# Performance work log

Measured on AMD Instinct MI355X. Metric: run time of the kernel, lower is better.

Reference implementation:

```python
import jax, jax.numpy as jnp
import numpy as np
import math

EMBED_DIM = 1024
NUM_HEADS = 16
HEAD_DIM = EMBED_DIM // NUM_HEADS
SEGMENT_LENGTHS = [2048, 4096]
DILATION_RATES = [1, 2]
B, N = 1, 8192
IS_CAUSAL = True


def setup_inputs() -> dict:
    key = jax.random.key(0)
    ks = jax.random.split(key, 12)
    def w(k):
        return (jax.random.normal(k, (EMBED_DIM, EMBED_DIM), dtype=jnp.float32) * 0.02)
    inp = {
        'query': jax.random.normal(ks[0], (B, N, EMBED_DIM), dtype=jnp.float32),
        'key':   jax.random.normal(ks[1], (B, N, EMBED_DIM), dtype=jnp.float32),
        'value': jax.random.normal(ks[2], (B, N, EMBED_DIM), dtype=jnp.float32),
        'Wq': w(ks[3]), 'bq': jnp.zeros((EMBED_DIM,), jnp.float32),
        'Wk': w(ks[4]), 'bk': jnp.zeros((EMBED_DIM,), jnp.float32),
        'Wv': w(ks[5]), 'bv': jnp.zeros((EMBED_DIM,), jnp.float32),
        'Wo': w(ks[6]), 'bo': jnp.zeros((EMBED_DIM,), jnp.float32),
    }
    return inp


def _dilated_group_attention(q, k, v, seg_len, dilation, offset, causal):
    # q,k,v: [B, N, Hg, D] -> dilated block attention within segments
    b, n, hg, d = q.shape
    nseg = n // seg_len
    m = seg_len // dilation  # dilated subsequence length per segment
    idx = offset + dilation * jnp.arange(m)  # positions inside a segment
    def gather(x):
        return x.reshape(b, nseg, seg_len, hg, d)[:, :, idx]  # [B,nseg,m,Hg,D]
    qs, ks_, vs = gather(q), gather(k), gather(v)
    scale = 1.0 / math.sqrt(d)
    # [B,nseg,Hg,m,m]
    scores = jnp.einsum('bnihd,bnjhd->bnhij', qs, ks_) * scale
    if causal:
        mask = jnp.tril(jnp.ones((m, m), dtype=bool))
        scores = jnp.where(mask, scores, jnp.finfo(scores.dtype).min)
    attn = jax.nn.softmax(scores, axis=-1)
    out = jnp.einsum('bnhij,bnjhd->bnihd', attn, vs)  # [B,nseg,m,Hg,D]
    # scatter dilated outputs back to full segment positions (others zero)
    full = jnp.zeros((b, nseg, seg_len, hg, d), dtype=out.dtype)
    full = full.at[:, :, idx].set(out)
    return full.reshape(b, n, hg, d)


def reference(query, key, value, Wq, bq, Wk, bk, Wv, bv, Wo, bo):
    b, n, e = query.shape
    q = query @ Wq.T + bq
    k = key @ Wk.T + bk
    v = value @ Wv.T + bv
    q = q.reshape(b, n, NUM_HEADS, HEAD_DIM)
    k = k.reshape(b, n, NUM_HEADS, HEAD_DIM)
    v = v.reshape(b, n, NUM_HEADS, HEAD_DIM)
    num_groups = len(SEGMENT_LENGTHS)
    hpg = NUM_HEADS // num_groups  # heads per (segment, dilation) group
    outs = []
    for g in range(num_groups):
        s, r = SEGMENT_LENGTHS[g], DILATION_RATES[g]
        off = g % r
        hsl = slice(g * hpg, (g + 1) * hpg)
        outs.append(_dilated_group_attention(q[:, :, hsl], k[:, :, hsl], v[:, :, hsl],
                                             s, r, off, IS_CAUSAL))
    attn_out = jnp.concatenate(outs, axis=2).reshape(b, n, e)
    return attn_out @ Wo.T + bo
```

## Files before the change

### kernel.cpp

```cpp
#include <hip/hip_runtime.h>
#include <hip/hip_bf16.h>

typedef __attribute__((ext_vector_type(8))) __bf16 bf16x8;
typedef __attribute__((ext_vector_type(8))) unsigned short us8;
typedef __attribute__((ext_vector_type(4))) float f32x4;
typedef __attribute__((ext_vector_type(16))) float f32x16;

#define N_TOK 8192
#define EMB 1024

static __device__ __forceinline__ unsigned short f2bf(float f) {
  union { __bf16 b; unsigned short u; } c;
  c.b = (__bf16)f;
  return c.u;
}

static __device__ __forceinline__ f32x4 mfma16(bf16x8 a, bf16x8 b, f32x4 c) {
  return __builtin_amdgcn_mfma_f32_16x16x32_bf16(a, b, c, 0, 0, 0);
}
static __device__ __forceinline__ f32x16 mfma32(bf16x8 a, bf16x8 b, f32x16 c) {
  return __builtin_amdgcn_mfma_f32_32x32x16_bf16(a, b, c, 0, 0, 0);
}
static __device__ __forceinline__ unsigned int cvtpk(float lo, float hi) {
  unsigned int r;
  asm("v_cvt_pk_bf16_f32 %0, %1, %2" : "=v"(r) : "v"(lo), "v"(hi));
  return r;
}

__global__ __launch_bounds__(256) void wconv(
    const float* __restrict__ W0, const float* __restrict__ W1,
    const float* __restrict__ W2, const float* __restrict__ W3,
    unsigned short* __restrict__ O)
{
  const float* W = (blockIdx.y == 0) ? W0 : (blockIdx.y == 1) ? W1 :
                   (blockIdx.y == 2) ? W2 : W3;
  unsigned short* o = O + (size_t)blockIdx.y * EMB * EMB;
  const int base = (blockIdx.x * 256 + threadIdx.x) * 16;
  float4 f0 = *(const float4*)(W + base);
  float4 f1 = *(const float4*)(W + base + 4);
  float4 f2 = *(const float4*)(W + base + 8);
  float4 f3 = *(const float4*)(W + base + 12);
  us8 p0, p1;
  p0[0]=f2bf(f0.x); p0[1]=f2bf(f0.y); p0[2]=f2bf(f0.z); p0[3]=f2bf(f0.w);
  p0[4]=f2bf(f1.x); p0[5]=f2bf(f1.y); p0[6]=f2bf(f1.z); p0[7]=f2bf(f1.w);
  p1[0]=f2bf(f2.x); p1[1]=f2bf(f2.y); p1[2]=f2bf(f2.z); p1[3]=f2bf(f2.w);
  p1[4]=f2bf(f3.x); p1[5]=f2bf(f3.y); p1[6]=f2bf(f3.z); p1[7]=f2bf(f3.w);
  *(us8*)(o + base)     = p0;
  *(us8*)(o + base + 8) = p1;
}

__global__ __launch_bounds__(256) void qkv_gemm3(
    const float* __restrict__ Xq, const float* __restrict__ Xk, const float* __restrict__ Xv,
    const unsigned short* __restrict__ Wb,
    const float* __restrict__ bq, const float* __restrict__ bk, const float* __restrict__ bv,
    unsigned short* __restrict__ O0, unsigned short* __restrict__ O1, unsigned short* __restrict__ O2)
{
  __shared__ __align__(16) unsigned short As[2][128][40];
  __shared__ __align__(16) unsigned short Bs[2][128][40];

  const int z = blockIdx.z;
  const float* X = (z == 0) ? Xq : (z == 1) ? Xk : Xv;
  const unsigned short* W = Wb + (size_t)z * EMB * EMB;
  const float* bias = (z == 0) ? bq : (z == 1) ? bk : bv;

  const int lin  = blockIdx.x;
  const int work = (lin & 7) * 64 + (lin >> 3);
  const long brow = (long)(work >> 3) * 128;
  const long bcol = (long)(work & 7) * 128;

  const int tid  = threadIdx.x;
  const int lane = tid & 63;
  const int wv   = tid >> 6;
  const int wrb  = (wv >> 1) * 64;
  const int wcb  = (wv & 1) * 64;

  const int srow = tid >> 1;
  const int skc  = (tid & 1) * 16;
  const int r16  = lane & 15;
  const int kq   = (lane >> 4) * 8;
  const int rq   = (lane >> 4) * 4;

  const float* Aaddr = X + (brow + srow) * (long)EMB + skc;
  const unsigned short* Baddr = W + (bcol + srow) * (long)EMB + skc;

  const f32x4 zz = {0.f, 0.f, 0.f, 0.f};
  f32x4 acc[4][4];
#pragma unroll
  for (int i = 0; i < 4; ++i)
#pragma unroll
    for (int j = 0; j < 4; ++j) acc[i][j] = zz;

  float4 a0 = *(const float4*)(Aaddr);
  float4 a1 = *(const float4*)(Aaddr + 4);
  float4 a2 = *(const float4*)(Aaddr + 8);
  float4 a3 = *(const float4*)(Aaddr + 12);
  us8 b0 = *(const us8*)(Baddr);
  us8 b1 = *(const us8*)(Baddr + 8);

  int p = 0;
  for (int k0 = 0; k0 < EMB; k0 += 32) {
    {
      us8 p0, p1;
      p0[0]=f2bf(a0.x); p0[1]=f2bf(a0.y); p0[2]=f2bf(a0.z); p0[3]=f2bf(a0.w);
      p0[4]=f2bf(a1.x); p0[5]=f2bf(a1.y); p0[6]=f2bf(a1.z); p0[7]=f2bf(a1.w);
      p1[0]=f2bf(a2.x); p1[1]=f2bf(a2.y); p1[2]=f2bf(a2.z); p1[3]=f2bf(a2.w);
      p1[4]=f2bf(a3.x); p1[5]=f2bf(a3.y); p1[6]=f2bf(a3.z); p1[7]=f2bf(a3.w);
      *(us8*)&As[p][srow][skc]     = p0;
      *(us8*)&As[p][srow][skc + 8] = p1;
      *(us8*)&Bs[p][srow][skc]     = b0;
      *(us8*)&Bs[p][srow][skc + 8] = b1;
    }
    if (k0 + 32 < EMB) {
      const float* An = Aaddr + k0 + 32;
      a0 = *(const float4*)(An);
      a1 = *(const float4*)(An + 4);
      a2 = *(const float4*)(An + 8);
      a3 = *(const float4*)(An + 12);
      const unsigned short* Bn = Baddr + k0 + 32;
      b0 = *(const us8*)(Bn);
      b1 = *(const us8*)(Bn + 8);
    }
    __syncthreads();

    bf16x8 av[4], bv_[4];
#pragma unroll
    for (int mi = 0; mi < 4; ++mi) av[mi]  = *(const bf16x8*)&As[p][wrb + mi*16 + r16][kq];
#pragma unroll
    for (int ni = 0; ni < 4; ++ni) bv_[ni] = *(const bf16x8*)&Bs[p][wcb + ni*16 + r16][kq];
#pragma unroll
    for (int mi = 0; mi < 4; ++mi)
#pragma unroll
      for (int ni = 0; ni < 4; ++ni)
        acc[mi][ni] = mfma16(av[mi], bv_[ni], acc[mi][ni]);
    p ^= 1;
  }

#pragma unroll
  for (int ni = 0; ni < 4; ++ni) {
    const long col = bcol + wcb + ni*16 + r16;
    const float bval = bias[col];
#pragma unroll
    for (int mi = 0; mi < 4; ++mi)
#pragma unroll
      for (int jr = 0; jr < 4; ++jr) {
        const long row = brow + wrb + mi*16 + rq + jr;
        const float v = acc[mi][ni][jr] + bval;
        if (z == 2) {
          long r = row;
          if (col >= 512) {
            const long seg = row >> 12;
            const long pp = row & 4095;
            r = (seg << 12) + ((pp & 1) ? (pp >> 1) : 2048 + (pp >> 1));
          }
          O2[col * (long)N_TOK + r] = f2bf(v);
        } else {
          unsigned short* O = (z == 0) ? O0 : O1;
          O[row * (long)EMB + col] = f2bf(v);
        }
      }
  }
}

__global__ __launch_bounds__(256) void attn_dilated3(
    const unsigned short* __restrict__ Qp, const unsigned short* __restrict__ Kp,
    const unsigned short* __restrict__ Vt, unsigned short* __restrict__ AO)
{
  __shared__ __align__(16) unsigned short Ks[2][64][72];
  __shared__ __align__(16) unsigned short Vs[2][64][72];

  const int z   = blockIdx.z;
  const int g1  = (z >= 4);
  const int dil = g1 ? 2 : 1;
  const int off = g1 ? 1 : 0;
  const long segb = g1 ? (long)(z - 4) * 4096 : (long)z * 2048;
  const int h   = (g1 ? 8 : 0) + blockIdx.y;
  const int h64 = h * 64;

  const int t    = 15 - (int)blockIdx.x;
  const int tid  = threadIdx.x;
  const int lane = tid & 63;
  const int w    = tid >> 6;
  const int q5   = lane & 31;
  const int hh   = lane >> 5;

  const int qq    = t*128 + w*32 + q5;
  const long qrow = segb + off + (long)dil * qq;

  bf16x8 qf[4];
  {
    const unsigned short* qsrc = Qp + qrow * EMB + h64 + 8*hh;
#pragma unroll
    for (int s = 0; s < 4; ++s) qf[s] = *(const bf16x8*)(qsrc + 16*s);
  }

  float m_run = -1e30f, l_run = 0.f;
  f32x16 o0, o1;
#pragma unroll
  for (int r = 0; r < 16; ++r) { o0[r] = 0.f; o1[r] = 0.f; }

  const int srow = tid >> 2;
  const int scs  = (tid & 3) * 16;
  const int jmax = 2*t + 1;
  const int jw   = (t*128 + w*32 + 31) >> 6;

  us8 kr0, kr1, vr0, vr1;
  {
    const long gk = segb + off + (long)dil * (0*64 + srow);
    const unsigned short* ksrc = Kp + gk*EMB + h64 + scs;
    kr0 = *(const us8*)ksrc; kr1 = *(const us8*)(ksrc + 8);
    const unsigned short* vsrc = Vt + (long)(h64 + srow)*N_TOK + segb + scs;
    vr0 = *(const us8*)vsrc; vr1 = *(const us8*)(vsrc + 8);
    *(us8*)&Ks[0][srow][scs]   = kr0;
    *(us8*)&Ks[0][srow][scs+8] = kr1;
    *(us8*)&Vs[0][srow][scs]   = vr0;
    *(us8*)&Vs[0][srow][scs+8] = vr1;
  }
  __syncthreads();
  int cur = 0;

  for (int j = 0; j <= jmax; ++j) {
    if (j < jmax) {
      const long gk = segb + off + (long)dil * ((j+1)*64 + srow);
      const unsigned short* ksrc = Kp + gk*EMB + h64 + scs;
      kr0 = *(const us8*)ksrc; kr1 = *(const us8*)(ksrc + 8);
      const unsigned short* vsrc = Vt + (long)(h64 + srow)*N_TOK + segb + (j+1)*64 + scs;
      vr0 = *(const us8*)vsrc; vr1 = *(const us8*)(vsrc + 8);
    }

    if (j <= jw) {
      f32x16 sa0, sa1;
#pragma unroll
      for (int r = 0; r < 16; ++r) { sa0[r] = 0.f; sa1[r] = 0.f; }
      __builtin_amdgcn_s_setprio(1);
#pragma unroll
      for (int s = 0; s < 4; ++s) {
        bf16x8 ka = *(const bf16x8*)&Ks[cur][q5][16*s + 8*hh];
        sa0 = mfma32(ka, qf[s], sa0);
      }
#pragma unroll
      for (int s = 0; s < 4; ++s) {
        bf16x8 kb = *(const bf16x8*)&Ks[cur][32 + q5][16*s + 8*hh];
        sa1 = mfma32(kb, qf[s], sa1);
      }
      __builtin_amdgcn_s_setprio(0);

      const bool do_kb1 = (j*64 + 32 <= t*128 + w*32 + 31);
      const bool diag   = (j*64 + 63 > t*128 + w*32);

      float sv[32];
      float mloc = -1e30f;
#pragma unroll
      for (int r = 0; r < 16; ++r) {
        const int kof = (r&3) + 8*(r>>2);
        float v = sa0[r] * 0.125f;
        if (diag && (j*64 + kof + 4*hh > qq)) v = -1e30f;
        sv[r] = v; mloc = fmaxf(mloc, v);
      }
      if (do_kb1) {
#pragma unroll
        for (int r = 0; r < 16; ++r) {
          const int kof = (r&3) + 8*(r>>2);
          float v = sa1[r] * 0.125f;
          if (diag && (j*64 + 32 + kof + 4*hh > qq)) v = -1e30f;
          sv[16+r] = v; mloc = fmaxf(mloc, v);
        }
      }
      mloc = fmaxf(mloc, __shfl_xor(mloc, 32, 64));

      const float mnew  = fmaxf(m_run, mloc);
      const float alpha = __expf(m_run - mnew);
      float psum = 0.f;
#pragma unroll
      for (int i = 0; i < 16; ++i) { float e = __expf(sv[i] - mnew); sv[i] = e; psum += e; }
      if (do_kb1) {
#pragma unroll
        for (int i = 16; i < 32; ++i) { float e = __expf(sv[i] - mnew); sv[i] = e; psum += e; }
      }
      psum += __shfl_xor(psum, 32, 64);
      l_run = l_run * alpha + psum;
      m_run = mnew;
#pragma unroll
      for (int r = 0; r < 16; ++r) { o0[r] *= alpha; o1[r] *= alpha; }

#pragma unroll
      for (int ks = 0; ks < 4; ++ks) {
        if (ks >= 2 && !do_kb1) continue;
        const unsigned int pk0 = cvtpk(sv[8*ks+0], sv[8*ks+1]);
        const unsigned int pk1 = cvtpk(sv[8*ks+2], sv[8*ks+3]);
        const unsigned int pk2 = cvtpk(sv[8*ks+4], sv[8*ks+5]);
        const unsigned int pk3 = cvtpk(sv[8*ks+6], sv[8*ks+7]);
        const unsigned int snd_lo = hh ? pk0 : pk2;
        const unsigned int snd_hi = hh ? pk1 : pk3;
        const unsigned int rcv_lo = (unsigned int)__shfl_xor((int)snd_lo, 32, 64);
        const unsigned int rcv_hi = (unsigned int)__shfl_xor((int)snd_hi, 32, 64);
        union { unsigned int wd[4]; bf16x8 v; } pu;
        pu.wd[0] = hh ? rcv_lo : pk0;
        pu.wd[1] = hh ? rcv_hi : pk1;
        pu.wd[2] = hh ? pk2 : rcv_lo;
        pu.wd[3] = hh ? pk3 : rcv_hi;
        __builtin_amdgcn_s_setprio(1);
        bf16x8 va = *(const bf16x8*)&Vs[cur][q5][16*ks + 8*hh];
        o0 = mfma32(va, pu.v, o0);
        bf16x8 vb = *(const bf16x8*)&Vs[cur][32 + q5][16*ks + 8*hh];
        o1 = mfma32(vb, pu.v, o1);
        __builtin_amdgcn_s_setprio(0);
      }
    }

    if (j < jmax) {
      *(us8*)&Ks[cur^1][srow][scs]   = kr0;
      *(us8*)&Ks[cur^1][srow][scs+8] = kr1;
      *(us8*)&Vs[cur^1][srow][scs]   = vr0;
      *(us8*)&Vs[cur^1][srow][scs+8] = vr1;
    }
    __syncthreads();
    cur ^= 1;
  }

  {
    const float inv = 1.f / l_run;
    unsigned short* dst = AO + qrow * EMB + h64;
#pragma unroll
    for (int r = 0; r < 16; ++r) {
      const int d = (r&3) + 8*(r>>2) + 4*hh;
      dst[d]      = f2bf(o0[r] * inv);
      dst[32 + d] = f2bf(o1[r] * inv);
    }
  }
}

__global__ __launch_bounds__(256) void gemm_out3(
    const unsigned short* __restrict__ A, const unsigned short* __restrict__ Wb,
    const float* __restrict__ bias, float* __restrict__ outp)
{
  __shared__ __align__(16) unsigned short As[2][128][40];
  __shared__ __align__(16) unsigned short Bs[2][128][40];

  const int lin  = blockIdx.x;
  const int work = (lin & 7) * 64 + (lin >> 3);
  const long brow = (long)(work >> 3) * 128;
  const long bcol = (long)(work & 7) * 128;

  const int tid  = threadIdx.x;
  const int lane = tid & 63;
  const int wv   = tid >> 6;
  const int wrb  = (wv >> 1) * 64;
  const int wcb  = (wv & 1) * 64;

  const int srow = tid >> 1;
  const int skc  = (tid & 1) * 16;
  const int r16  = lane & 15;
  const int kq   = (lane >> 4) * 8;
  const int rq   = (lane >> 4) * 4;

  const unsigned short* Aaddr = A  + (brow + srow) * (long)EMB + skc;
  const unsigned short* Baddr = Wb + (bcol + srow) * (long)EMB + skc;

  const f32x4 zz = {0.f, 0.f, 0.f, 0.f};
  f32x4 acc[4][4];
#pragma unroll
  for (int i = 0; i < 4; ++i)
#pragma unroll
    for (int j = 0; j < 4; ++j) acc[i][j] = zz;

  us8 a0 = *(const us8*)(Aaddr);
  us8 a1 = *(const us8*)(Aaddr + 8);
  us8 b0 = *(const us8*)(Baddr);
  us8 b1 = *(const us8*)(Baddr + 8);

  int p = 0;
  for (int k0 = 0; k0 < EMB; k0 += 32) {
    *(us8*)&As[p][srow][skc]     = a0;
    *(us8*)&As[p][srow][skc + 8] = a1;
    *(us8*)&Bs[p][srow][skc]     = b0;
    *(us8*)&Bs[p][srow][skc + 8] = b1;
    if (k0 + 32 < EMB) {
      a0 = *(const us8*)(Aaddr + k0 + 32);
      a1 = *(const us8*)(Aaddr + k0 + 40);
      b0 = *(const us8*)(Baddr + k0 + 32);
      b1 = *(const us8*)(Baddr + k0 + 40);
    }
    __syncthreads();

    bf16x8 av[4], bv_[4];
#pragma unroll
    for (int mi = 0; mi < 4; ++mi) av[mi]  = *(const bf16x8*)&As[p][wrb + mi*16 + r16][kq];
#pragma unroll
    for (int ni = 0; ni < 4; ++ni) bv_[ni] = *(const bf16x8*)&Bs[p][wcb + ni*16 + r16][kq];
#pragma unroll
    for (int mi = 0; mi < 4; ++mi)
#pragma unroll
      for (int ni = 0; ni < 4; ++ni)
        acc[mi][ni] = mfma16(av[mi], bv_[ni], acc[mi][ni]);
    p ^= 1;
  }

#pragma unroll
  for (int ni = 0; ni < 4; ++ni) {
    const long col = bcol + wcb + ni*16 + r16;
    const float bval = bias[col];
#pragma unroll
    for (int mi = 0; mi < 4; ++mi)
#pragma unroll
      for (int jr = 0; jr < 4; ++jr) {
        const long row = brow + wrb + mi*16 + rq + jr;
        outp[row * (long)EMB + col] = acc[mi][ni][jr] + bval;
      }
  }
}

extern "C" void kernel_launch(void* const* d_in, const int* in_sizes, int n_in,
                              void* d_out, int out_size, void* d_ws, size_t ws_size,
                              hipStream_t stream) {
  const float* query = (const float*)d_in[0];
  const float* key_  = (const float*)d_in[1];
  const float* value = (const float*)d_in[2];
  const float* Wq = (const float*)d_in[3];
  const float* bq = (const float*)d_in[4];
  const float* Wk = (const float*)d_in[5];
  const float* bk = (const float*)d_in[6];
  const float* Wv = (const float*)d_in[7];
  const float* bv = (const float*)d_in[8];
  const float* Wo = (const float*)d_in[9];
  const float* bo = (const float*)d_in[10];

  unsigned short* Qp  = (unsigned short*)d_ws;
  unsigned short* Kp  = Qp + (size_t)N_TOK * EMB;
  unsigned short* Vt  = Kp + (size_t)N_TOK * EMB;
  unsigned short* AO  = Vt + (size_t)N_TOK * EMB;
  unsigned short* Wb  = AO + (size_t)N_TOK * EMB;
  unsigned short* Wob = Wb + (size_t)3 * EMB * EMB;

  dim3 blk(256);

  hipLaunchKernelGGL(wconv, dim3(EMB*EMB/(256*16), 4), blk, 0, stream,
                     Wq, Wk, Wv, Wo, Wb);

  hipLaunchKernelGGL(qkv_gemm3, dim3(512, 1, 3), blk, 0, stream,
                     query, key_, value, Wb, bq, bk, bv, Qp, Kp, Vt);

  hipMemsetAsync(AO, 0, (size_t)N_TOK * EMB * 2, stream);

  hipLaunchKernelGGL(attn_dilated3, dim3(16, 8, 6), blk, 0, stream, Qp, Kp, Vt, AO);

  hipLaunchKernelGGL(gemm_out3, dim3(512), blk, 0, stream, AO, Wob, bo, (float*)d_out);
}
```

Before: 232.9 us.

## Pre-convert inputs to bf16 and stage GEMM tiles via direct global-to-LDS loads

Folds the fp32-to-bf16 conversion of the query/key/value activations into the weight-conversion kernel, writing the bf16 copies into scratch space borrowed from the output buffer and workspace. Both the QKV and output GEMMs now fill LDS with global_load_lds 16-byte transfers instead of register staging, using an unpadded single-buffered tile with two barriers per k-step. This removes conversion work and register traffic from the GEMM inner loop, at the cost of an extra full pass over the activations. It also drops the double-buffer prefetch overlap and the LDS padding, so bank conflicts and exposed load latency may increase.

New measurement: 251.9 us. +8.1%, slower.

```diff
diff --git a/kernel.cpp b/kernel.cpp
--- a/kernel.cpp
+++ b/kernel.cpp
@@ -26,40 +26,61 @@
   asm("v_cvt_pk_bf16_f32 %0, %1, %2" : "=v"(r) : "v"(lo), "v"(hi));
   return r;
 }
-
-__global__ __launch_bounds__(256) void wconv(
+static __device__ __forceinline__ void gload16(const unsigned short* g, unsigned short* l) {
+  __builtin_amdgcn_global_load_lds(
+      (const __attribute__((address_space(1))) unsigned int*)g,
+      (__attribute__((address_space(3))) unsigned int*)l, 16, 0, 0);
+}
+
+__global__ __launch_bounds__(256) void convall(
+    const float* __restrict__ X0, const float* __restrict__ X1, const float* __restrict__ X2,
     const float* __restrict__ W0, const float* __restrict__ W1,
     const float* __restrict__ W2, const float* __restrict__ W3,
-    unsigned short* __restrict__ O)
+    unsigned short* __restrict__ Dq, unsigned short* __restrict__ Dk,
+    unsigned short* __restrict__ Dv, unsigned short* __restrict__ Wb)
 {
-  const float* W = (blockIdx.y == 0) ? W0 : (blockIdx.y == 1) ? W1 :
-                   (blockIdx.y == 2) ? W2 : W3;
-  unsigned short* o = O + (size_t)blockIdx.y * EMB * EMB;
-  const int base = (blockIdx.x * 256 + threadIdx.x) * 16;
-  float4 f0 = *(const float4*)(W + base);
-  float4 f1 = *(const float4*)(W + base + 4);
-  float4 f2 = *(const float4*)(W + base + 8);
-  float4 f3 = *(const float4*)(W + base + 12);
+  const int bid = blockIdx.x;
+  const float* src;
+  unsigned short* dst;
+  long base;
+  if (bid < 6144) {
+    const int t = bid >> 11;
+    const int b = bid & 2047;
+    src = (t == 0) ? X0 : (t == 1) ? X1 : X2;
+    dst = (t == 0) ? Dq : (t == 1) ? Dk : Dv;
+    base = ((long)b * 256 + threadIdx.x) * 16;
+  } else {
+    const int r = bid - 6144;
+    const int t = r >> 8;
+    const int b = r & 255;
+    src = (t == 0) ? W0 : (t == 1) ? W1 : (t == 2) ? W2 : W3;
+    dst = Wb + (size_t)t * EMB * EMB;
+    base = ((long)b * 256 + threadIdx.x) * 16;
+  }
+  float4 f0 = *(const float4*)(src + base);
+  float4 f1 = *(const float4*)(src + base + 4);
+  float4 f2 = *(const float4*)(src + base + 8);
+  float4 f3 = *(const float4*)(src + base + 12);
   us8 p0, p1;
   p0[0]=f2bf(f0.x); p0[1]=f2bf(f0.y); p0[2]=f2bf(f0.z); p0[3]=f2bf(f0.w);
   p0[4]=f2bf(f1.x); p0[5]=f2bf(f1.y); p0[6]=f2bf(f1.z); p0[7]=f2bf(f1.w);
   p1[0]=f2bf(f2.x); p1[1]=f2bf(f2.y); p1[2]=f2bf(f2.z); p1[3]=f2bf(f2.w);
   p1[4]=f2bf(f3.x); p1[5]=f2bf(f3.y); p1[6]=f2bf(f3.z); p1[7]=f2bf(f3.w);
-  *(us8*)(o + base)     = p0;
-  *(us8*)(o + base + 8) = p1;
-}
-
-__global__ __launch_bounds__(256) void qkv_gemm3(
-    const float* __restrict__ Xq, const float* __restrict__ Xk, const float* __restrict__ Xv,
-    const unsigned short* __restrict__ Wb,
+  *(us8*)(dst + base)     = p0;
+  *(us8*)(dst + base + 8) = p1;
+}
+
+__global__ __launch_bounds__(256) void qkv_gemm4(
+    const unsigned short* __restrict__ Xq, const unsigned short* __restrict__ Xk,
+    const unsigned short* __restrict__ Xv, const unsigned short* __restrict__ Wb,
     const float* __restrict__ bq, const float* __restrict__ bk, const float* __restrict__ bv,
     unsigned short* __restrict__ O0, unsigned short* __restrict__ O1, unsigned short* __restrict__ O2)
 {
-  __shared__ __align__(16) unsigned short As[2][128][40];
-  __shared__ __align__(16) unsigned short Bs[2][128][40];
+  __shared__ __align__(16) unsigned short As[128 * 32];
+  __shared__ __align__(16) unsigned short Bs[128 * 32];
 
   const int z = blockIdx.z;
-  const float* X = (z == 0) ? Xq : (z == 1) ? Xk : Xv;
+  const unsigned short* X = (z == 0) ? Xq : (z == 1) ? Xk : Xv;
   const unsigned short* W = Wb + (size_t)z * EMB * EMB;
   const float* bias = (z == 0) ? bq : (z == 1) ? bk : bv;
 
@@ -70,18 +91,23 @@
 
   const int tid  = threadIdx.x;
   const int lane = tid & 63;
-  const int wv   = tid >> 6;
-  const int wrb  = (wv >> 1) * 64;
-  const int wcb  = (wv & 1) * 64;
-
-  const int srow = tid >> 1;
-  const int skc  = (tid & 1) * 16;
+  const int w    = tid >> 6;
+  const int wrb  = (w >> 1) * 64;
+  const int wcb  = (w & 1) * 64;
   const int r16  = lane & 15;
   const int kq   = (lane >> 4) * 8;
   const int rq   = (lane >> 4) * 4;
 
-  const float* Aaddr = X + (brow + srow) * (long)EMB + skc;
-  const unsigned short* Baddr = W + (bcol + srow) * (long)EMB + skc;
+  const int srow = lane >> 2;
+  const int scol = (lane & 3) * 8;
+  const unsigned short* Ag0 = X + (brow + w*32      + srow) * (long)EMB + scol;
+  const unsigned short* Ag1 = X + (brow + w*32 + 16 + srow) * (long)EMB + scol;
+  const unsigned short* Bg0 = W + (bcol + w*32      + srow) * (long)EMB + scol;
+  const unsigned short* Bg1 = W + (bcol + w*32 + 16 + srow) * (long)EMB + scol;
+  unsigned short* Al0 = As + w * 1024;
+  unsigned short* Al1 = As + w * 1024 + 512;
+  unsigned short* Bl0 = Bs + w * 1024;
+  unsigned short* Bl1 = Bs + w * 1024 + 512;
 
   const f32x4 zz = {0.f, 0.f, 0.f, 0.f};
   f32x4 acc[4][4];
@@ -90,49 +116,24 @@
 #pragma unroll
     for (int j = 0; j < 4; ++j) acc[i][j] = zz;
 
-  float4 a0 = *(const float4*)(Aaddr);
-  float4 a1 = *(const float4*)(Aaddr + 4);
-  float4 a2 = *(const float4*)(Aaddr + 8);
-  float4 a3 = *(const float4*)(Aaddr + 12);
-  us8 b0 = *(const us8*)(Baddr);
-  us8 b1 = *(const us8*)(Baddr + 8);
-
-  int p = 0;
   for (int k0 = 0; k0 < EMB; k0 += 32) {
-    {
-      us8 p0, p1;
-      p0[0]=f2bf(a0.x); p0[1]=f2bf(a0.y); p0[2]=f2bf(a0.z); p0[3]=f2bf(a0.w);
-      p0[4]=f2bf(a1.x); p0[5]=f2bf(a1.y); p0[6]=f2bf(a1.z); p0[7]=f2bf(a1.w);
-      p1[0]=f2bf(a2.x); p1[1]=f2bf(a2.y); p1[2]=f2bf(a2.z); p1[3]=f2bf(a2.w);
-      p1[4]=f2bf(a3.x); p1[5]=f2bf(a3.y); p1[6]=f2bf(a3.z); p1[7]=f2bf(a3.w);
-      *(us8*)&As[p][srow][skc]     = p0;
-      *(us8*)&As[p][srow][skc + 8] = p1;
-      *(us8*)&Bs[p][srow][skc]     = b0;
-      *(us8*)&Bs[p][srow][skc + 8] = b1;
-    }
-    if (k0 + 32 < EMB) {
-      const float* An = Aaddr + k0 + 32;
-      a0 = *(const float4*)(An);
-      a1 = *(const float4*)(An + 4);
-      a2 = *(const float4*)(An + 8);
-      a3 = *(const float4*)(An + 12);
-      const unsigned short* Bn = Baddr + k0 + 32;
-      b0 = *(const us8*)(Bn);
-      b1 = *(const us8*)(Bn + 8);
-    }
     __syncthreads();
+    gload16(Ag0 + k0, Al0);
+    gload16(Ag1 + k0, Al1);
+    gload16(Bg0 + k0, Bl0);
+    gload16(Bg1 + k0, Bl1);
+    __syncthreads();
 
     bf16x8 av[4], bv_[4];
 #pragma unroll
-    for (int mi = 0; mi < 4; ++mi) av[mi]  = *(const bf16x8*)&As[p][wrb + mi*16 + r16][kq];
-#pragma unroll
-    for (int ni = 0; ni < 4; ++ni) bv_[ni] = *(const bf16x8*)&Bs[p][wcb + ni*16 + r16][kq];
+    for (int mi = 0; mi < 4; ++mi) av[mi]  = *(const bf16x8*)&As[(wrb + mi*16 + r16)*32 + kq];
+#pragma unroll
+    for (int ni = 0; ni < 4; ++ni) bv_[ni] = *(const bf16x8*)&Bs[(wcb + ni*16 + r16)*32 + kq];
 #pragma unroll
     for (int mi = 0; mi < 4; ++mi)
 #pragma unroll
       for (int ni = 0; ni < 4; ++ni)
         acc[mi][ni] = mfma16(av[mi], bv_[ni], acc[mi][ni]);
-    p ^= 1;
   }
 
 #pragma unroll
@@ -329,12 +330,12 @@
   }
 }
 
-__global__ __launch_bounds__(256) void gemm_out3(
+__global__ __launch_bounds__(256) void gemm_out4(
     const unsigned short* __restrict__ A, const unsigned short* __restrict__ Wb,
     const float* __restrict__ bias, float* __restrict__ outp)
 {
-  __shared__ __align__(16) unsigned short As[2][128][40];
-  __shared__ __align__(16) unsigned short Bs[2][128][40];
+  __shared__ __align__(16) unsigned short As[128 * 32];
+  __shared__ __align__(16) unsigned short Bs[128 * 32];
 
   const int lin  = blockIdx.x;
   const int work = (lin & 7) * 64 + (lin >> 3);
@@ -343,18 +344,23 @@
 
   const int tid  = threadIdx.x;
   const int lane = tid & 63;
-  const int wv   = tid >> 6;
-  const int wrb  = (wv >> 1) * 64;
-  const int wcb  = (wv & 1) * 64;
-
-  const int srow = tid >> 1;
-  const int skc  = (tid & 1) * 16;
+  const int w    = tid >> 6;
+  const int wrb  = (w >> 1) * 64;
+  const int wcb  = (w & 1) * 64;
   const int r16  = lane & 15;
   const int kq   = (lane >> 4) * 8;
   const int rq   = (lane >> 4) * 4;
 
-  const unsigned short* Aaddr = A  + (brow + srow) * (long)EMB + skc;
-  const unsigned short* Baddr = Wb + (bcol + srow) * (long)EMB + skc;
+  const int srow = lane >> 2;
+  const int scol = (lane & 3) * 8;
+  const unsigned short* Ag0 = A  + (brow + w*32      + srow) * (long)EMB + scol;
+  const unsigned short* Ag1 = A  + (brow + w*32 + 16 + srow) * (long)EMB + scol;
+  const unsigned short* Bg0 = Wb + (bcol + w*32      + srow) * (long)EMB + scol;
+  const unsigned short* Bg1 = Wb + (bcol + w*32 + 16 + srow) * (long)EMB + scol;
+  unsigned short* Al0 = As + w * 1024;
+  unsigned short* Al1 = As + w * 1024 + 512;
+  unsigned short* Bl0 = Bs + w * 1024;
+  unsigned short* Bl1 = Bs + w * 1024 + 512;
 
   const f32x4 zz = {0.f, 0.f, 0.f, 0.f};
   f32x4 acc[4][4];
@@ -363,36 +369,24 @@
 #pragma unroll
     for (int j = 0; j < 4; ++j) acc[i][j] = zz;
 
-  us8 a0 = *(const us8*)(Aaddr);
-  us8 a1 = *(const us8*)(Aaddr + 8);
-  us8 b0 = *(const us8*)(Baddr);
-  us8 b1 = *(const us8*)(Baddr + 8);
-
-  int p = 0;
   for (int k0 = 0; k0 < EMB; k0 += 32) {
-    *(us8*)&As[p][srow][skc]     = a0;
-    *(us8*)&As[p][srow][skc + 8] = a1;
-    *(us8*)&Bs[p][srow][skc]     = b0;
-    *(us8*)&Bs[p][srow][skc + 8] = b1;
-    if (k0 + 32 < EMB) {
-      a0 = *(const us8*)(Aaddr + k0 + 32);
-      a1 = *(const us8*)(Aaddr + k0 + 40);
-      b0 = *(const us8*)(Baddr + k0 + 32);
-      b1 = *(const us8*)(Baddr + k0 + 40);
-    }
     __syncthreads();
+    gload16(Ag0 + k0, Al0);
+    gload16(Ag1 + k0, Al1);
+    gload16(Bg0 + k0, Bl0);
+    gload16(Bg1 + k0, Bl1);
+    __syncthreads();
 
     bf16x8 av[4], bv_[4];
 #pragma unroll
-    for (int mi = 0; mi < 4; ++mi) av[mi]  = *(const bf16x8*)&As[p][wrb + mi*16 + r16][kq];
-#pragma unroll
-    for (int ni = 0; ni < 4; ++ni) bv_[ni] = *(const bf16x8*)&Bs[p][wcb + ni*16 + r16][kq];
+    for (int mi = 0; mi < 4; ++mi) av[mi]  = *(const bf16x8*)&As[(wrb + mi*16 + r16)*32 + kq];
+#pragma unroll
+    for (int ni = 0; ni < 4; ++ni) bv_[ni] = *(const bf16x8*)&Bs[(wcb + ni*16 + r16)*32 + kq];
 #pragma unroll
     for (int mi = 0; mi < 4; ++mi)
 #pragma unroll
       for (int ni = 0; ni < 4; ++ni)
         acc[mi][ni] = mfma16(av[mi], bv_[ni], acc[mi][ni]);
-    p ^= 1;
   }
 
 #pragma unroll
@@ -427,21 +421,25 @@
   unsigned short* Qp  = (unsigned short*)d_ws;
   unsigned short* Kp  = Qp + (size_t)N_TOK * EMB;
   unsigned short* Vt  = Kp + (size_t)N_TOK * EMB;
-  unsigned short* AO  = Vt + (size_t)N_TOK * EMB;
-  unsigned short* Wb  = AO + (size_t)N_TOK * EMB;
+  unsigned short* Wb  = Vt + (size_t)N_TOK * EMB;
+  unsigned short* S   = Wb + (size_t)4 * EMB * EMB;
+  unsigned short* Xbq = (unsigned short*)d_out;
+  unsigned short* Xbk = Xbq + (size_t)N_TOK * EMB;
+  unsigned short* Xbv = S;
+  unsigned short* AO  = S;
   unsigned short* Wob = Wb + (size_t)3 * EMB * EMB;
 
   dim3 blk(256);
 
-  hipLaunchKernelGGL(wconv, dim3(EMB*EMB/(256*16), 4), blk, 0, stream,
-                     Wq, Wk, Wv, Wo, Wb);
-
-  hipLaunchKernelGGL(qkv_gemm3, dim3(512, 1, 3), blk, 0, stream,
-                     query, key_, value, Wb, bq, bk, bv, Qp, Kp, Vt);
+  hipLaunchKernelGGL(convall, dim3(7168), blk, 0, stream,
+                     query, key_, value, Wq, Wk, Wv, Wo, Xbq, Xbk, Xbv, Wb);
+
+  hipLaunchKernelGGL(qkv_gemm4, dim3(512, 1, 3), blk, 0, stream,
+                     Xbq, Xbk, Xbv, Wb, bq, bk, bv, Qp, Kp, Vt);
 
   hipMemsetAsync(AO, 0, (size_t)N_TOK * EMB * 2, stream);
 
   hipLaunchKernelGGL(attn_dilated3, dim3(16, 8, 6), blk, 0, stream, Qp, Kp, Vt, AO);
 
-  hipLaunchKernelGGL(gemm_out3, dim3(512), blk, 0, stream, AO, Wob, bo, (float*)d_out);
-}
+  hipLaunchKernelGGL(gemm_out4, dim3(512), blk, 0, stream, AO, Wob, bo, (float*)d_out);
+}
```
